# Performance work log

Measured on AMD Instinct MI355X. Metric: run time of the kernel, lower is better.

The kernel has to match this reference:

```python
import jax, jax.numpy as jnp
import numpy as np

EPS = 1e-7  # K.epsilon()

def setup_inputs() -> dict:
    key = jax.random.key(0)
    k1, k2, k3 = jax.random.split(key, 3)
    B, T, D = 32, 2048, 512
    x = jax.random.normal(k1, (B, T, D), dtype=jnp.float32)
    W = jax.random.normal(k2, (D, D), dtype=jnp.float32) * (1.0 / np.sqrt(D))
    b = jnp.zeros((D,), dtype=jnp.float32)
    u = jax.random.normal(k3, (D,), dtype=jnp.float32) * (1.0 / np.sqrt(D))
    return {"x": x, "W": W, "b": b, "u": u}

def reference(x, W, b, u):
    # uit = tanh(x @ W + b)  -> [B, T, D]
    uit = jnp.tanh(jnp.einsum('btd,de->bte', x, W) + b)
    # scores: sum over feature dim of uit * u -> [B, T]
    ait = jnp.einsum('btd,d->bt', uit, u)
    # exp + normalize over T (no mask); matches original exp/sum form
    a = jnp.exp(ait)
    a = a / (jnp.sum(a, axis=1, keepdims=True) + EPS)
    # weighted sum pooling over T -> [B, D]
    return jnp.einsum('btd,bt->bd', x, a)
```

## Files before the change

### kernel.cpp

```cpp
#include <hip/hip_runtime.h>
#include <math.h>

#define D_DIM 512

typedef short short8v __attribute__((ext_vector_type(8)));
typedef unsigned short ushort8v __attribute__((ext_vector_type(8)));
typedef unsigned short ushort4v __attribute__((ext_vector_type(4)));
typedef float f32x16 __attribute__((ext_vector_type(16)));

__device__ inline unsigned short f2bf(float f) {
    union { float f; unsigned int u; } a; a.f = f;
    unsigned int u = a.u;
    unsigned int r = (u + 0x7fffu + ((u >> 16) & 1u)) >> 16;
    return (unsigned short)r;
}

__device__ inline float fast_tanh(float y) {
    float e2 = __expf(2.f * y);
    return 1.f - __fdividef(2.f, e2 + 1.f);
}

#define ASYNC_CP16(gp, lp) \
    __builtin_amdgcn_global_load_lds( \
        (const __attribute__((address_space(1))) void*)(gp), \
        (__attribute__((address_space(3))) void*)(lp), 16, 0, 0)

__global__ __launch_bounds__(1024) void wt_kernel(const float* __restrict__ W,
                                                  unsigned short* __restrict__ Wb2,
                                                  float* __restrict__ zero_base,
                                                  int zero_count) {
    __shared__ __align__(16) unsigned short lbuf[16384];
    const int s = blockIdx.x;
    const int tid = threadIdx.x;
    if (s == 0) {
        for (int i = tid; i < zero_count; i += 1024) zero_base[i] = 0.f;
    }
    #pragma unroll
    for (int i = 0; i < 4; ++i) {
        int flat = tid + i * 1024;
        int kr = flat >> 7;
        int e4 = (flat & 127) * 4;
        float4 v = *(const float4*)(W + (size_t)(s * 32 + kr) * D_DIM + e4);
        int ks = kr >> 4, half = (kr >> 3) & 1, j = kr & 7;
        float vv[4] = {v.x, v.y, v.z, v.w};
        #pragma unroll
        for (int q = 0; q < 4; ++q) {
            int e = e4 + q, nt = e >> 5, nl = e & 31;
            lbuf[(((nt * 2 + ks) * 2 + half) * 32 + nl) * 8 + j] = f2bf(vv[q]);
        }
    }
    __syncthreads();
    #pragma unroll
    for (int i = 0; i < 2; ++i) {
        int c = tid + i * 1024;
        *(ushort8v*)(Wb2 + (size_t)s * 16384 + c * 8) = *(const ushort8v*)&lbuf[c * 8];
    }
}

constexpr int XLDE = 40;

__global__ __launch_bounds__(512, 4) void gemm_ait_fused(
    const float* __restrict__ x, const unsigned short* __restrict__ Wb2,
    const float* __restrict__ bias, const float* __restrict__ u,
    float* __restrict__ numer, float* __restrict__ denom, int T)
{
    __shared__ __align__(16) unsigned short wsh[2][16384];
    __shared__ __align__(16) unsigned short xs[2][64 * XLDE];
    __shared__ float rowpart[8][64];

    const int tid  = threadIdx.x;
    const int wave = tid >> 6;
    const int lane = tid & 63;
    const int half = lane >> 5;
    const int nl   = lane & 31;
    const int m0   = blockIdx.x * 64;

    f32x16 acc[2][2];
    #pragma unroll
    for (int mi = 0; mi < 2; ++mi)
        #pragma unroll
        for (int ni = 0; ni < 2; ++ni)
            #pragma unroll
            for (int r = 0; r < 16; ++r) acc[mi][ni][r] = 0.f;

    const int xr  = tid >> 3;
    const int xc4 = tid & 7;
    const float* xbase = x + (size_t)(m0 + xr) * D_DIM + xc4 * 4;

    #pragma unroll
    for (int i = 0; i < 4; ++i)
        ASYNC_CP16(Wb2 + tid * 8 + i * 4096, &wsh[0][tid * 8 + i * 4096]);
    float4 px = *(const float4*)(xbase);

    for (int s = 0; s < 16; ++s) {
        const int pb = s & 1;
        {
            ushort4v pk;
            pk[0] = f2bf(px.x); pk[1] = f2bf(px.y);
            pk[2] = f2bf(px.z); pk[3] = f2bf(px.w);
            *(ushort4v*)&xs[pb][xr * XLDE + xc4 * 4] = pk;
        }
        __syncthreads();

        if (s + 1 < 16) {
            const unsigned short* wsrc = Wb2 + (size_t)(s + 1) * 16384;
            #pragma unroll
            for (int i = 0; i < 4; ++i)
                ASYNC_CP16(wsrc + tid * 8 + i * 4096, &wsh[1 - pb][tid * 8 + i * 4096]);
            px = *(const float4*)(xbase + (s + 1) * 32);
        }

        #pragma unroll
        for (int ks = 0; ks < 2; ++ks) {
            short8v af[2], bfr[2];
            #pragma unroll
            for (int mi = 0; mi < 2; ++mi)
                af[mi] = *(const short8v*)&xs[pb][(mi * 32 + nl) * XLDE + ks * 16 + half * 8];
            #pragma unroll
            for (int ni = 0; ni < 2; ++ni)
                bfr[ni] = *(const short8v*)&wsh[pb][(((wave * 2 + ni) * 2 + ks) * 2 + half) * 256 + nl * 8];
            #pragma unroll
            for (int mi = 0; mi < 2; ++mi)
                #pragma unroll
                for (int ni = 0; ni < 2; ++ni)
                    acc[mi][ni] = __builtin_amdgcn_mfma_f32_32x32x16_bf16(
                        af[mi], bfr[ni], acc[mi][ni], 0, 0, 0);
        }
    }

    float rowsum[2][16];
    #pragma unroll
    for (int mi = 0; mi < 2; ++mi)
        #pragma unroll
        for (int r = 0; r < 16; ++r) rowsum[mi][r] = 0.f;

    #pragma unroll
    for (int mi = 0; mi < 2; ++mi) {
        #pragma unroll
        for (int ni = 0; ni < 2; ++ni) {
            int col = wave * 64 + ni * 32 + nl;
            float be = bias[col], ue = u[col];
            #pragma unroll
            for (int r = 0; r < 16; ++r)
                rowsum[mi][r] += fast_tanh(acc[mi][ni][r] + be) * ue;
        }
    }
    #pragma unroll
    for (int mi = 0; mi < 2; ++mi)
        #pragma unroll
        for (int r = 0; r < 16; ++r) {
            float v = rowsum[mi][r];
            v += __shfl_xor(v, 1, 64);
            v += __shfl_xor(v, 2, 64);
            v += __shfl_xor(v, 4, 64);
            v += __shfl_xor(v, 8, 64);
            v += __shfl_xor(v, 16, 64);
            rowsum[mi][r] = v;
        }
    if (nl == 0) {
        #pragma unroll
        for (int mi = 0; mi < 2; ++mi)
            #pragma unroll
            for (int r = 0; r < 16; ++r) {
                int row = mi * 32 + (r & 3) + 8 * (r >> 2) + 4 * half;
                rowpart[wave][row] = rowsum[mi][r];
            }
    }
    __syncthreads();

    const int b = m0 / T;
    float* evals = (float*)&xs[0][0];
    if (tid < 64) {
        float s = 0.f;
        #pragma unroll
        for (int w = 0; w < 8; ++w) s += rowpart[w][tid];
        float e = __expf(s);
        evals[tid] = e;
        float t = e;
        t += __shfl_xor(t, 1, 64);
        t += __shfl_xor(t, 2, 64);
        t += __shfl_xor(t, 4, 64);
        t += __shfl_xor(t, 8, 64);
        t += __shfl_xor(t, 16, 64);
        t += __shfl_xor(t, 32, 64);
        if (tid == 0) atomicAdd(denom + b, t);
    }
    __syncthreads();

    const int dg = tid >> 7;
    const int d4 = (tid & 127) << 2;
    const float* xp = x + (size_t)m0 * D_DIM + d4;
    float4 pacc = {0.f, 0.f, 0.f, 0.f};
    #pragma unroll 4
    for (int r = dg; r < 64; r += 4) {
        float e = evals[r];
        float4 xv = *(const float4*)(xp + (size_t)r * D_DIM);
        pacc.x += e * xv.x; pacc.y += e * xv.y;
        pacc.z += e * xv.z; pacc.w += e * xv.w;
    }
    float4* ptmp = (float4*)&wsh[0][0];
    if (dg > 0) ptmp[(dg - 1) * 128 + (tid & 127)] = pacc;
    __syncthreads();
    if (dg == 0) {
        float4 o0 = ptmp[tid], o1 = ptmp[128 + tid], o2 = ptmp[256 + tid];
        float* np = numer + (size_t)b * D_DIM + d4;
        atomicAdd(np + 0, pacc.x + o0.x + o1.x + o2.x);
        atomicAdd(np + 1, pacc.y + o0.y + o1.y + o2.y);
        atomicAdd(np + 2, pacc.z + o0.z + o1.z + o2.z);
        atomicAdd(np + 3, pacc.w + o0.w + o1.w + o2.w);
    }
}

__global__ __launch_bounds__(128) void out_div_kernel(
    const float* __restrict__ numer, const float* __restrict__ denom,
    float* __restrict__ out)
{
    const int b = blockIdx.x;
    const int tid = threadIdx.x;
    float inv = 1.0f / (denom[b] + 1e-7f);
    float4 v = *(const float4*)(numer + (size_t)b * D_DIM + tid * 4);
    v.x *= inv; v.y *= inv; v.z *= inv; v.w *= inv;
    *(float4*)(out + (size_t)b * D_DIM + tid * 4) = v;
}

__global__ __launch_bounds__(256) void gemm_ait_f32(
    const float* __restrict__ x, const float* __restrict__ W,
    const float* __restrict__ bias, const float* __restrict__ u,
    float* __restrict__ ait)
{
    __shared__ float xsf[64][68];
    __shared__ float wshf[64][132];
    const int tid = threadIdx.x;
    const int tx = tid & 15, ty = tid >> 4;
    const int m0 = blockIdx.x * 64;
    float rowsum[4] = {0.f, 0.f, 0.f, 0.f};
    for (int e0 = 0; e0 < D_DIM; e0 += 128) {
        float acc[4][8];
        #pragma unroll
        for (int i = 0; i < 4; ++i)
            #pragma unroll
            for (int j = 0; j < 8; ++j) acc[i][j] = 0.f;
        for (int kc = 0; kc < D_DIM; kc += 64) {
            #pragma unroll
            for (int i = 0; i < 4; ++i) {
                int idx = tid + i * 256;
                int r = idx >> 4, c = (idx & 15) * 4;
                *(float4*)&xsf[r][c] = *(const float4*)(x + (size_t)(m0 + r) * D_DIM + kc + c);
            }
            #pragma unroll
            for (int i = 0; i < 8; ++i) {
                int idx = tid + i * 256;
                int r = idx >> 5, c = (idx & 31) * 4;
                *(float4*)&wshf[r][c] = *(const float4*)(W + (size_t)(kc + r) * D_DIM + e0 + c);
            }
            __syncthreads();
            #pragma unroll 4
            for (int k = 0; k < 64; ++k) {
                float xv[4];
                #pragma unroll
                for (int i = 0; i < 4; ++i) xv[i] = xsf[ty * 4 + i][k];
                float4 w0 = *(const float4*)&wshf[k][tx * 8];
                float4 w1 = *(const float4*)&wshf[k][tx * 8 + 4];
                #pragma unroll
                for (int i = 0; i < 4; ++i) {
                    acc[i][0] += xv[i] * w0.x; acc[i][1] += xv[i] * w0.y;
                    acc[i][2] += xv[i] * w0.z; acc[i][3] += xv[i] * w0.w;
                    acc[i][4] += xv[i] * w1.x; acc[i][5] += xv[i] * w1.y;
                    acc[i][6] += xv[i] * w1.z; acc[i][7] += xv[i] * w1.w;
                }
            }
            __syncthreads();
        }
        #pragma unroll
        for (int j = 0; j < 8; ++j) {
            int e = e0 + tx * 8 + j;
            float be = bias[e], ue = u[e];
            #pragma unroll
            for (int i = 0; i < 4; ++i) rowsum[i] += tanhf(acc[i][j] + be) * ue;
        }
    }
    float* red = &xsf[0][0];
    #pragma unroll
    for (int i = 0; i < 4; ++i) red[(ty * 4 + i) * 16 + tx] = rowsum[i];
    __syncthreads();
    if (tid < 64) {
        float s = 0.f;
        #pragma unroll
        for (int j = 0; j < 16; ++j) s += red[tid * 16 + j];
        ait[m0 + tid] = s;
    }
}

__global__ __launch_bounds__(256) void softmax_kernel(float* __restrict__ ait, int T)
{
    const int b = blockIdx.x;
    float* p = ait + (size_t)b * T;
    const int tid = threadIdx.x;
    float ev[8];
    float local = 0.f;
    #pragma unroll
    for (int i = 0; i < 8; ++i) {
        ev[i] = expf(p[tid + i * 256]);
        local += ev[i];
    }
    #pragma unroll
    for (int off = 32; off > 0; off >>= 1)
        local += __shfl_down(local, off, 64);
    __shared__ float wsum[4];
    const int wv = tid >> 6, lane = tid & 63;
    if (lane == 0) wsum[wv] = local;
    __syncthreads();
    float total = wsum[0] + wsum[1] + wsum[2] + wsum[3];
    float inv = 1.0f / (total + 1e-7f);
    #pragma unroll
    for (int i = 0; i < 8; ++i) p[tid + i * 256] = ev[i] * inv;
}

__global__ __launch_bounds__(256) void pool_atomic_kernel(
    const float* __restrict__ x, const float* __restrict__ a,
    float* __restrict__ out, int T)
{
    const int chunks = T >> 8;
    const int b = blockIdx.x / chunks;
    const int c = blockIdx.x % chunks;
    const int tid = threadIdx.x;
    const int th = tid >> 7;
    const int d = (tid & 127) * 4;
    const float* xp = x + ((size_t)b * T + c * 256) * D_DIM + d;
    const float* ap = a + (size_t)b * T + c * 256;
    float4 acc = {0.f, 0.f, 0.f, 0.f};
    #pragma unroll 8
    for (int t = th; t < 256; t += 2) {
        float s = ap[t];
        float4 xv = *(const float4*)(xp + (size_t)t * D_DIM);
        acc.x += xv.x * s; acc.y += xv.y * s;
        acc.z += xv.z * s; acc.w += xv.w * s;
    }
    __shared__ float4 tmp[128];
    if (th == 1) tmp[tid & 127] = acc;
    __syncthreads();
    if (th == 0) {
        float4 o = tmp[tid];
        float* op = out + (size_t)b * D_DIM + tid * 4;
        atomicAdd(op + 0, acc.x + o.x);
        atomicAdd(op + 1, acc.y + o.y);
        atomicAdd(op + 2, acc.z + o.z);
        atomicAdd(op + 3, acc.w + o.w);
    }
}

extern "C" void kernel_launch(void* const* d_in, const int* in_sizes, int n_in,
                              void* d_out, int out_size, void* d_ws, size_t ws_size,
                              hipStream_t stream)
{
    const float* x    = (const float*)d_in[0];
    const float* W    = (const float*)d_in[1];
    const float* bias = (const float*)d_in[2];
    const float* u    = (const float*)d_in[3];
    float* out = (float*)d_out;

    const int Dd = in_sizes[2];
    const int M  = in_sizes[0] / Dd;
    const int B  = out_size / Dd;
    const int T  = M / B;
    const int chunks = T >> 8;

    const size_t wb_bytes  = (size_t)Dd * Dd * sizeof(unsigned short);
    const size_t ait_bytes = (size_t)M * sizeof(float);

    if (ws_size >= wb_bytes + ait_bytes) {
        unsigned short* Wb2 = (unsigned short*)d_ws;
        float* numer = (float*)((char*)d_ws + wb_bytes);
        float* denom = numer + (size_t)B * Dd;
        const int zero_count = B * Dd + B;

        wt_kernel<<<dim3(16), dim3(1024), 0, stream>>>(W, Wb2, numer, zero_count);
        gemm_ait_fused<<<dim3(M / 64), dim3(512), 0, stream>>>(x, Wb2, bias, u,
                                                               numer, denom, T);
        out_div_kernel<<<dim3(B), dim3(128), 0, stream>>>(numer, denom, out);
    } else {
        float* ait = (float*)d_ws;
        gemm_ait_f32<<<dim3(M / 64), dim3(256), 0, stream>>>(x, W, bias, u, ait);
        softmax_kernel<<<dim3(B), dim3(256), 0, stream>>>(ait, T);
        hipMemsetAsync(d_out, 0, (size_t)out_size * sizeof(float), stream);
        pool_atomic_kernel<<<dim3(B * chunks), dim3(256), 0, stream>>>(x, ait, out, T);
    }
}
```

Measured before the change: 242.1 us.

## Deepen GEMM K-pipeline to prefetch distance two with finer K steps and inline asm

Splits the K loop into 32 steps of 16 instead of 16 steps of 32. W now uses a 4-deep LDS ring and x a 3-deep ring, so both are prefetched two steps ahead, with explicit vmcnt/lgkmcnt waits, raw s_barrier and sched_barrier fences. The weight pre-layout is reorganised to match, the x row stride shrinks, and loads and LDS reads are written as inline asm. The aim is to hide global latency better and avoid compiler-inserted full waits, at the cost of twice as many barriers per tile and fragile hand-counted wait values.

```diff
diff --git a/kernel.cpp b/kernel.cpp
--- a/kernel.cpp
+++ b/kernel.cpp
@@ -5,7 +5,6 @@
 
 typedef short short8v __attribute__((ext_vector_type(8)));
 typedef unsigned short ushort8v __attribute__((ext_vector_type(8)));
-typedef unsigned short ushort4v __attribute__((ext_vector_type(4)));
 typedef float f32x16 __attribute__((ext_vector_type(16)));
 
 __device__ inline unsigned short f2bf(float f) {
@@ -24,6 +23,10 @@
     __builtin_amdgcn_global_load_lds( \
         (const __attribute__((address_space(1))) void*)(gp), \
         (__attribute__((address_space(3))) void*)(lp), 16, 0, 0)
+
+__device__ inline unsigned ldsaddr(const void* p) {
+    return (unsigned)(size_t)(__attribute__((address_space(3))) const void*)p;
+}
 
 __global__ __launch_bounds__(1024) void wt_kernel(const float* __restrict__ W,
                                                   unsigned short* __restrict__ Wb2,
@@ -45,8 +48,8 @@
         float vv[4] = {v.x, v.y, v.z, v.w};
         #pragma unroll
         for (int q = 0; q < 4; ++q) {
-            int e = e4 + q, nt = e >> 5, nl = e & 31;
-            lbuf[(((nt * 2 + ks) * 2 + half) * 32 + nl) * 8 + j] = f2bf(vv[q]);
+            int e = e4 + q, g = e >> 5, nl = e & 31;
+            lbuf[ks * 8192 + ((g * 2 + half) * 32 + nl) * 8 + j] = f2bf(vv[q]);
         }
     }
     __syncthreads();
@@ -57,15 +60,15 @@
     }
 }
 
-constexpr int XLDE = 40;
+constexpr int XLDE = 24;
 
 __global__ __launch_bounds__(512, 4) void gemm_ait_fused(
     const float* __restrict__ x, const unsigned short* __restrict__ Wb2,
     const float* __restrict__ bias, const float* __restrict__ u,
     float* __restrict__ numer, float* __restrict__ denom, int T)
 {
-    __shared__ __align__(16) unsigned short wsh[2][16384];
-    __shared__ __align__(16) unsigned short xs[2][64 * XLDE];
+    __shared__ __align__(16) unsigned short wsh[4][8192];
+    __shared__ __align__(16) unsigned short xs[3][64 * XLDE];
     __shared__ float rowpart[8][64];
 
     const int tid  = threadIdx.x;
@@ -83,49 +86,68 @@
             #pragma unroll
             for (int r = 0; r < 16; ++r) acc[mi][ni][r] = 0.f;
 
-    const int xr  = tid >> 3;
-    const int xc4 = tid & 7;
-    const float* xbase = x + (size_t)(m0 + xr) * D_DIM + xc4 * 4;
-
-    #pragma unroll
-    for (int i = 0; i < 4; ++i)
-        ASYNC_CP16(Wb2 + tid * 8 + i * 4096, &wsh[0][tid * 8 + i * 4096]);
-    float4 px = *(const float4*)(xbase);
-
-    for (int s = 0; s < 16; ++s) {
-        const int pb = s & 1;
+    const int xr = tid >> 3;
+    const int kp = tid & 7;
+    const float* xb = x + (size_t)(m0 + xr) * D_DIM + kp * 2;
+
+    float2 pxr[2];
+
+    asm volatile("global_load_dwordx2 %0, %1, off" : "=v"(pxr[0]) : "v"(xb));
+    ASYNC_CP16(Wb2 + tid * 8,        &wsh[0][tid * 8]);
+    ASYNC_CP16(Wb2 + tid * 8 + 4096, &wsh[0][tid * 8 + 4096]);
+    asm volatile("global_load_dwordx2 %0, %1, off" : "=v"(pxr[1]) : "v"(xb + 16));
+    ASYNC_CP16(Wb2 + 8192 + tid * 8,        &wsh[1][tid * 8]);
+    ASYNC_CP16(Wb2 + 8192 + tid * 8 + 4096, &wsh[1][tid * 8 + 4096]);
+    asm volatile("s_waitcnt vmcnt(5)" ::: "memory");
+    __builtin_amdgcn_sched_barrier(0);
+    {
+        unsigned int pk = (unsigned int)f2bf(pxr[0].x) | ((unsigned int)f2bf(pxr[0].y) << 16);
+        *(unsigned int*)&xs[0][xr * XLDE + kp * 2] = pk;
+    }
+
+    #pragma unroll
+    for (int s = 0; s < 32; ++s) {
+        if (s + 2 < 32) {
+            asm volatile("global_load_dwordx2 %0, %1, off"
+                         : "=v"(pxr[s & 1]) : "v"(xb + (s + 2) * 16));
+            ASYNC_CP16(Wb2 + (size_t)(s + 2) * 8192 + tid * 8,
+                       &wsh[(s + 2) & 3][tid * 8]);
+            ASYNC_CP16(Wb2 + (size_t)(s + 2) * 8192 + tid * 8 + 4096,
+                       &wsh[(s + 2) & 3][tid * 8 + 4096]);
+            asm volatile("s_waitcnt vmcnt(5)" ::: "memory");
+        } else if (s == 30) {
+            asm volatile("s_waitcnt vmcnt(2)" ::: "memory");
+        } else {
+            asm volatile("s_waitcnt vmcnt(0)" ::: "memory");
+        }
+        __builtin_amdgcn_sched_barrier(0);
+        if (s + 1 < 32) {
+            float2 p = pxr[(s + 1) & 1];
+            unsigned int pk = (unsigned int)f2bf(p.x) | ((unsigned int)f2bf(p.y) << 16);
+            *(unsigned int*)&xs[(s + 1) % 3][xr * XLDE + kp * 2] = pk;
+        }
+        asm volatile("s_waitcnt lgkmcnt(0)" ::: "memory");
+        __builtin_amdgcn_s_barrier();
+        __builtin_amdgcn_sched_barrier(0);
+
+        short8v af0, af1, bf0, bf1;
         {
-            ushort4v pk;
-            pk[0] = f2bf(px.x); pk[1] = f2bf(px.y);
-            pk[2] = f2bf(px.z); pk[3] = f2bf(px.w);
-            *(ushort4v*)&xs[pb][xr * XLDE + xc4 * 4] = pk;
-        }
-        __syncthreads();
-
-        if (s + 1 < 16) {
-            const unsigned short* wsrc = Wb2 + (size_t)(s + 1) * 16384;
-            #pragma unroll
-            for (int i = 0; i < 4; ++i)
-                ASYNC_CP16(wsrc + tid * 8 + i * 4096, &wsh[1 - pb][tid * 8 + i * 4096]);
-            px = *(const float4*)(xbase + (s + 1) * 32);
-        }
-
-        #pragma unroll
-        for (int ks = 0; ks < 2; ++ks) {
-            short8v af[2], bfr[2];
-            #pragma unroll
-            for (int mi = 0; mi < 2; ++mi)
-                af[mi] = *(const short8v*)&xs[pb][(mi * 32 + nl) * XLDE + ks * 16 + half * 8];
-            #pragma unroll
-            for (int ni = 0; ni < 2; ++ni)
-                bfr[ni] = *(const short8v*)&wsh[pb][(((wave * 2 + ni) * 2 + ks) * 2 + half) * 256 + nl * 8];
-            #pragma unroll
-            for (int mi = 0; mi < 2; ++mi)
-                #pragma unroll
-                for (int ni = 0; ni < 2; ++ni)
-                    acc[mi][ni] = __builtin_amdgcn_mfma_f32_32x32x16_bf16(
-                        af[mi], bfr[ni], acc[mi][ni], 0, 0, 0);
-        }
+            unsigned a0 = ldsaddr(&xs[s % 3][(nl) * XLDE + half * 8]);
+            unsigned a1 = ldsaddr(&xs[s % 3][(32 + nl) * XLDE + half * 8]);
+            unsigned b0 = ldsaddr(&wsh[s & 3][(((wave * 2 + 0) * 2 + half) * 32 + nl) * 8]);
+            unsigned b1 = ldsaddr(&wsh[s & 3][(((wave * 2 + 1) * 2 + half) * 32 + nl) * 8]);
+            asm volatile("ds_read_b128 %0, %1" : "=v"(af0) : "v"(a0) : "memory");
+            asm volatile("ds_read_b128 %0, %1" : "=v"(af1) : "v"(a1) : "memory");
+            asm volatile("ds_read_b128 %0, %1" : "=v"(bf0) : "v"(b0) : "memory");
+            asm volatile("ds_read_b128 %0, %1" : "=v"(bf1) : "v"(b1) : "memory");
+        }
+        asm volatile("s_waitcnt lgkmcnt(0)" ::: "memory");
+        __builtin_amdgcn_sched_barrier(0);
+
+        acc[0][0] = __builtin_amdgcn_mfma_f32_32x32x16_bf16(af0, bf0, acc[0][0], 0, 0, 0);
+        acc[0][1] = __builtin_amdgcn_mfma_f32_32x32x16_bf16(af0, bf1, acc[0][1], 0, 0, 0);
+        acc[1][0] = __builtin_amdgcn_mfma_f32_32x32x16_bf16(af1, bf0, acc[1][0], 0, 0, 0);
+        acc[1][1] = __builtin_amdgcn_mfma_f32_32x32x16_bf16(af1, bf1, acc[1][1], 0, 0, 0);
     }
 
     float rowsum[2][16];
```

New measurement: 239.2 us. No clear change (-1.2%).

## Stream W fragments directly to registers and stage full x tile in LDS

Applied to the files above, without the earlier changes.

The GEMM main loop is restructured. The whole 64x512 x tile is converted to bf16 once and stored in LDS in MFMA-fragment order. Each wave now loads its W fragments straight from global memory into registers with inline-asm loads, double-buffered two steps ahead, instead of staging W through shared memory. This removes the per-step __syncthreads and the W LDS round-trip, and hand-manages waitcnt and sched barriers plus setprio around the MFMAs. In exchange, each workgroup uses 64KB of LDS and occupancy hint drops to 2, and the inline-asm waitcnt accounting is fragile.

```diff
diff --git a/kernel.cpp b/kernel.cpp
--- a/kernel.cpp
+++ b/kernel.cpp
@@ -20,10 +20,9 @@
     return 1.f - __fdividef(2.f, e2 + 1.f);
 }
 
-#define ASYNC_CP16(gp, lp) \
-    __builtin_amdgcn_global_load_lds( \
-        (const __attribute__((address_space(1))) void*)(gp), \
-        (__attribute__((address_space(3))) void*)(lp), 16, 0, 0)
+__device__ inline unsigned ldsaddr(const void* p) {
+    return (unsigned)(size_t)(__attribute__((address_space(3))) const void*)p;
+}
 
 __global__ __launch_bounds__(1024) void wt_kernel(const float* __restrict__ W,
                                                   unsigned short* __restrict__ Wb2,
@@ -45,8 +44,8 @@
         float vv[4] = {v.x, v.y, v.z, v.w};
         #pragma unroll
         for (int q = 0; q < 4; ++q) {
-            int e = e4 + q, nt = e >> 5, nl = e & 31;
-            lbuf[(((nt * 2 + ks) * 2 + half) * 32 + nl) * 8 + j] = f2bf(vv[q]);
+            int e = e4 + q, g = e >> 5, nl = e & 31;
+            lbuf[ks * 8192 + ((g * 2 + half) * 32 + nl) * 8 + j] = f2bf(vv[q]);
         }
     }
     __syncthreads();
@@ -57,15 +56,12 @@
     }
 }
 
-constexpr int XLDE = 40;
-
-__global__ __launch_bounds__(512, 4) void gemm_ait_fused(
+__global__ __launch_bounds__(512, 2) void gemm_ait_fused(
     const float* __restrict__ x, const unsigned short* __restrict__ Wb2,
     const float* __restrict__ bias, const float* __restrict__ u,
     float* __restrict__ numer, float* __restrict__ denom, int T)
 {
-    __shared__ __align__(16) unsigned short wsh[2][16384];
-    __shared__ __align__(16) unsigned short xs[2][64 * XLDE];
+    __shared__ __align__(16) unsigned short xa[32768];
     __shared__ float rowpart[8][64];
 
     const int tid  = threadIdx.x;
@@ -83,48 +79,66 @@
             #pragma unroll
             for (int r = 0; r < 16; ++r) acc[mi][ni][r] = 0.f;
 
-    const int xr  = tid >> 3;
-    const int xc4 = tid & 7;
-    const float* xbase = x + (size_t)(m0 + xr) * D_DIM + xc4 * 4;
-
-    #pragma unroll
-    for (int i = 0; i < 4; ++i)
-        ASYNC_CP16(Wb2 + tid * 8 + i * 4096, &wsh[0][tid * 8 + i * 4096]);
-    float4 px = *(const float4*)(xbase);
-
-    for (int s = 0; s < 16; ++s) {
-        const int pb = s & 1;
-        {
-            ushort4v pk;
-            pk[0] = f2bf(px.x); pk[1] = f2bf(px.y);
-            pk[2] = f2bf(px.z); pk[3] = f2bf(px.w);
-            *(ushort4v*)&xs[pb][xr * XLDE + xc4 * 4] = pk;
-        }
-        __syncthreads();
-
-        if (s + 1 < 16) {
-            const unsigned short* wsrc = Wb2 + (size_t)(s + 1) * 16384;
-            #pragma unroll
-            for (int i = 0; i < 4; ++i)
-                ASYNC_CP16(wsrc + tid * 8 + i * 4096, &wsh[1 - pb][tid * 8 + i * 4096]);
-            px = *(const float4*)(xbase + (s + 1) * 32);
-        }
-
-        #pragma unroll
-        for (int ks = 0; ks < 2; ++ks) {
-            short8v af[2], bfr[2];
-            #pragma unroll
-            for (int mi = 0; mi < 2; ++mi)
-                af[mi] = *(const short8v*)&xs[pb][(mi * 32 + nl) * XLDE + ks * 16 + half * 8];
-            #pragma unroll
-            for (int ni = 0; ni < 2; ++ni)
-                bfr[ni] = *(const short8v*)&wsh[pb][(((wave * 2 + ni) * 2 + ks) * 2 + half) * 256 + nl * 8];
-            #pragma unroll
-            for (int mi = 0; mi < 2; ++mi)
-                #pragma unroll
-                for (int ni = 0; ni < 2; ++ni)
-                    acc[mi][ni] = __builtin_amdgcn_mfma_f32_32x32x16_bf16(
-                        af[mi], bfr[ni], acc[mi][ni], 0, 0, 0);
+    short8v a[2][2], b[2][2];
+
+    const unsigned bvoff0 = (unsigned)(((wave * 4 + half) * 32 + nl) * 16);
+
+    asm volatile("global_load_dwordx4 %0, %1, %2"
+                 : "=v"(b[0][0]) : "v"(bvoff0), "s"(Wb2) : "memory");
+    asm volatile("global_load_dwordx4 %0, %1, %2 offset:1024"
+                 : "=v"(b[0][1]) : "v"(bvoff0), "s"(Wb2) : "memory");
+    {
+        unsigned v1 = bvoff0 + 16384u;
+        asm volatile("global_load_dwordx4 %0, %1, %2"
+                     : "=v"(b[1][0]) : "v"(v1), "s"(Wb2) : "memory");
+        asm volatile("global_load_dwordx4 %0, %1, %2 offset:1024"
+                     : "=v"(b[1][1]) : "v"(v1), "s"(Wb2) : "memory");
+    }
+
+    #pragma unroll
+    for (int i = 0; i < 16; ++i) {
+        int flat = tid + i * 512;
+        int row = flat >> 7;
+        int c4  = (flat & 127) * 4;
+        float4 v = *(const float4*)(x + (size_t)(m0 + row) * D_DIM + c4);
+        int ks = c4 >> 4, hf = (c4 >> 3) & 1, j0 = c4 & 7;
+        int mi = row >> 5, r5 = row & 31;
+        ushort4v pk;
+        pk[0] = f2bf(v.x); pk[1] = f2bf(v.y); pk[2] = f2bf(v.z); pk[3] = f2bf(v.w);
+        *(ushort4v*)&xa[(((ks * 2 + mi) * 2 + hf) * 32 + r5) * 8 + j0] = pk;
+    }
+    __syncthreads();
+
+    const unsigned abase = ldsaddr(&xa[0]) + (unsigned)(half * 512 + nl * 16);
+    asm volatile("ds_read_b128 %0, %1" : "=v"(a[0][0]) : "v"(abase) : "memory");
+    asm volatile("ds_read_b128 %0, %1 offset:1024" : "=v"(a[0][1]) : "v"(abase) : "memory");
+
+    #pragma unroll
+    for (int s = 0; s < 32; ++s) {
+        if (s < 31) { asm volatile("s_waitcnt vmcnt(2)" ::: "memory"); }
+        else        { asm volatile("s_waitcnt vmcnt(0)" ::: "memory"); }
+        __builtin_amdgcn_sched_barrier(0);
+        if (s + 1 < 32) {
+            unsigned ao = abase + (unsigned)((s + 1) * 2048);
+            asm volatile("ds_read_b128 %0, %1" : "=v"(a[(s + 1) & 1][0]) : "v"(ao) : "memory");
+            asm volatile("ds_read_b128 %0, %1 offset:1024" : "=v"(a[(s + 1) & 1][1]) : "v"(ao) : "memory");
+            asm volatile("s_waitcnt lgkmcnt(2)" ::: "memory");
+        } else {
+            asm volatile("s_waitcnt lgkmcnt(0)" ::: "memory");
+        }
+        __builtin_amdgcn_sched_barrier(0);
+        __builtin_amdgcn_s_setprio(1);
+        acc[0][0] = __builtin_amdgcn_mfma_f32_32x32x16_bf16(a[s & 1][0], b[s & 1][0], acc[0][0], 0, 0, 0);
+        acc[0][1] = __builtin_amdgcn_mfma_f32_32x32x16_bf16(a[s & 1][0], b[s & 1][1], acc[0][1], 0, 0, 0);
+        acc[1][0] = __builtin_amdgcn_mfma_f32_32x32x16_bf16(a[s & 1][1], b[s & 1][0], acc[1][0], 0, 0, 0);
+        acc[1][1] = __builtin_amdgcn_mfma_f32_32x32x16_bf16(a[s & 1][1], b[s & 1][1], acc[1][1], 0, 0, 0);
+        __builtin_amdgcn_s_setprio(0);
+        if (s + 2 < 32) {
+            unsigned vo = bvoff0 + (unsigned)((s + 2) * 16384);
+            asm volatile("global_load_dwordx4 %0, %1, %2"
+                         : "=v"(b[s & 1][0]) : "v"(vo), "s"(Wb2) : "memory");
+            asm volatile("global_load_dwordx4 %0, %1, %2 offset:1024"
+                         : "=v"(b[s & 1][1]) : "v"(vo), "s"(Wb2) : "memory");
         }
     }
 
@@ -168,8 +182,8 @@
     }
     __syncthreads();
 
-    const int b = m0 / T;
-    float* evals = (float*)&xs[0][0];
+    const int bidx = m0 / T;
+    float* evals = (float*)&xa[0];
     if (tid < 64) {
         float s = 0.f;
         #pragma unroll
@@ -183,7 +197,7 @@
         t += __shfl_xor(t, 8, 64);
         t += __shfl_xor(t, 16, 64);
         t += __shfl_xor(t, 32, 64);
-        if (tid == 0) atomicAdd(denom + b, t);
+        if (tid == 0) atomicAdd(denom + bidx, t);
     }
     __syncthreads();
 
@@ -198,12 +212,12 @@
         pacc.x += e * xv.x; pacc.y += e * xv.y;
         pacc.z += e * xv.z; pacc.w += e * xv.w;
     }
-    float4* ptmp = (float4*)&wsh[0][0];
+    float4* ptmp = (float4*)&xa[256];
     if (dg > 0) ptmp[(dg - 1) * 128 + (tid & 127)] = pacc;
     __syncthreads();
     if (dg == 0) {
         float4 o0 = ptmp[tid], o1 = ptmp[128 + tid], o2 = ptmp[256 + tid];
-        float* np = numer + (size_t)b * D_DIM + d4;
+        float* np = numer + (size_t)bidx * D_DIM + d4;
         atomicAdd(np + 0, pacc.x + o0.x + o1.x + o2.x);
         atomicAdd(np + 1, pacc.y + o0.y + o1.y + o2.y);
         atomicAdd(np + 2, pacc.z + o0.z + o1.z + o2.z);
```

Result: no change. 243.8 us (+0.7%).
